# Optimization experiments

Hardware: AMD Instinct MI355X
Metric: run time of the kernel (lower is better)

## Reference

```python
import jax, jax.numpy as jnp
import numpy as np

B, N, H = 32, 1024, 128
EPS = 1e-5


def setup_inputs() -> dict:
    key = jax.random.key(0)
    ks = jax.random.split(key, 9)
    node_embeddings = jax.random.normal(ks[0], (B, N, H), dtype=jnp.float32)
    edge_relations = jax.random.normal(ks[1], (B, N, N, 3), dtype=jnp.float32)
    adjacency = jax.random.randint(ks[2], (N, N), 0, 2, dtype=jnp.int32)
    s_msg = 1.0 / np.sqrt(H + 3)
    s_upd = 1.0 / np.sqrt(2 * H)
    W_msg = jax.random.uniform(ks[3], (H, H + 3), jnp.float32, -s_msg, s_msg)
    b_msg = jax.random.uniform(ks[4], (H,), jnp.float32, -s_msg, s_msg)
    W_upd = jax.random.uniform(ks[5], (H, 2 * H), jnp.float32, -s_upd, s_upd)
    b_upd = jax.random.uniform(ks[6], (H,), jnp.float32, -s_upd, s_upd)
    gamma = jnp.ones((H,), jnp.float32)
    beta = jnp.zeros((H,), jnp.float32)
    return {"node_embeddings": node_embeddings, "edge_relations": edge_relations,
            "adjacency": adjacency, "W_msg": W_msg, "b_msg": b_msg,
            "W_upd": W_upd, "b_upd": b_upd, "gamma": gamma, "beta": beta}


def reference(node_embeddings, edge_relations, adjacency, W_msg, b_msg, W_upd, b_upd, gamma, beta):
    # node_embeddings: [B,N,H]; edge_relations: [B,N,N,3]; adjacency: [N,N]
    b_, n_, h_ = node_embeddings.shape
    mask = (adjacency > 0).astype(node_embeddings.dtype)  # mask[j,i]=1 if i is neighbor of j
    # Split msg_nn weight: Linear(cat(h_i, e_ij)) = h_i @ W_h^T + e_ij @ W_e^T + b
    W_h = W_msg[:, :h_]   # [H,H]
    W_e = W_msg[:, h_:]   # [H,3]
    h_part = jnp.einsum('bih,oh->bio', node_embeddings, W_h)       # [B,N,H]
    msg_h = jnp.einsum('ji,bio->bjo', mask, h_part)                # aggregate sender linear part
    e_agg = jnp.einsum('bijc,ji->bjc', edge_relations, mask)       # aggregate edge feats first (memory-bound)
    msg_e = jnp.einsum('bjc,oc->bjo', e_agg, W_e)
    deg = mask.sum(axis=1)                                         # [N] in-degree of j
    messages = msg_h + msg_e + deg[None, :, None] * b_msg          # bias added once per edge
    # Dropout(0.2) is identity in inference; BatchNorm uses batch stats (training-mode math).
    upd_in = jnp.concatenate([node_embeddings, messages], axis=-1)  # [B,N,2H]
    updated = jax.nn.relu(jnp.einsum('bjk,ok->bjo', upd_in, W_upd) + b_upd)
    flat = updated.reshape(-1, h_)
    mean = flat.mean(axis=0)
    var = flat.var(axis=0)  # biased, as BatchNorm1d
    normed = (flat - mean) * jax.lax.rsqrt(var + EPS) * gamma + beta
    return normed.reshape(b_, n_, h_) + node_embeddings
```

## Files before the change

kernel.cpp:

```cpp
#include <hip/hip_runtime.h>
#include <hip/hip_bf16.h>

typedef _Float16 f16;
typedef f16 f16x4 __attribute__((ext_vector_type(4)));
typedef f16 f16x8 __attribute__((ext_vector_type(8)));
typedef float f32x4 __attribute__((ext_vector_type(4)));

#define BB 32
#define NN 1024
#define HH 128
#define ROWS (BB*NN)
#define EPS 1e-5f

__device__ __forceinline__ f16 f2h(float x) { return (f16)x; }

__global__ __launch_bounds__(256) void prep0_k(
    const float* __restrict__ W_msg, const float* __restrict__ W_upd,
    f16* __restrict__ Wh, f16* __restrict__ Wupd, float* __restrict__ We,
    float* __restrict__ e_agg, float* __restrict__ deg, float* __restrict__ sums)
{
  const int blk = blockIdx.x, t = threadIdx.x;
  if (blk == 0) {
    for (int idx = t; idx < HH*HH; idx += 256) {
      const int o = idx >> 7, h = idx & 127;
      Wh[idx] = f2h(W_msg[o*131 + h]);
    }
  } else if (blk == 1) {
    for (int idx = t; idx < HH*256; idx += 256)
      Wupd[idx] = f2h(W_upd[idx]);
  } else if (blk == 2) {
    for (int idx = t; idx < HH*3; idx += 256)
      We[idx] = W_msg[(idx/3)*131 + 128 + (idx % 3)];
    if (t < 256) sums[t] = 0.f;
    for (int idx = t; idx < NN; idx += 256) deg[idx] = 0.f;
  } else {
    const int base = (blk - 3) * 24576 + t;
    #pragma unroll
    for (int r = 0; r < 96; r++) e_agg[base + r*256] = 0.f;
  }
}

__global__ __launch_bounds__(256) void phaseB_k(
    const float* __restrict__ node, const float* __restrict__ E,
    const int* __restrict__ adj, const f16* __restrict__ Wh,
    f16* __restrict__ h_part_T, float* __restrict__ e_agg,
    float* __restrict__ deg)
{
  __shared__ f16 As[128*32];
  __shared__ f16 Bs[128*32];
  const int tid = threadIdx.x;

  if (blockIdx.x >= 256) {
    const int e  = blockIdx.x - 256;
    const int bb = e >> 5;
    const int r5 = e & 31;
    const int jt = r5 & 3;
    const int ih = r5 >> 2;
    const int j  = (jt << 8) + tid;
    const int i0 = ih << 7;
    const float* Ep = E + (long)bb*3145728 + (long)i0*3072 + (long)j*3;
    const int*   Ap = adj + (long)j*NN + i0;
    float a0 = 0.f, a1 = 0.f, a2 = 0.f, dc = 0.f;
    for (int ii = 0; ii < 128; ii += 8) {
      const int4 m0 = *(const int4*)(Ap + ii);
      const int4 m1 = *(const int4*)(Ap + ii + 4);
      float ev[8][3];
      #pragma unroll
      for (int v = 0; v < 8; v++) {
        const float* q = Ep + (long)(ii + v)*3072;
        ev[v][0] = q[0]; ev[v][1] = q[1]; ev[v][2] = q[2];
      }
      const int mm[8] = {m0.x, m0.y, m0.z, m0.w, m1.x, m1.y, m1.z, m1.w};
      #pragma unroll
      for (int v = 0; v < 8; v++) {
        const float m = (mm[v] > 0) ? 1.f : 0.f;
        a0 = fmaf(m, ev[v][0], a0);
        a1 = fmaf(m, ev[v][1], a1);
        a2 = fmaf(m, ev[v][2], a2);
        dc += m;
      }
    }
    const long eb = ((long)bb*NN + j)*3;
    atomicAdd(&e_agg[eb],     a0);
    atomicAdd(&e_agg[eb + 1], a1);
    atomicAdd(&e_agg[eb + 2], a2);
    if (bb == 0) atomicAdd(&deg[j], dc);
    return;
  }

  const int g  = blockIdx.x;
  const int nt = g & 7, bb = g >> 3;
  const int nbase = nt << 7;
  const int lane = tid & 63, wave = tid >> 6;
  const int wm = (wave & 1) << 6, wn = (wave >> 1) << 6;

  f32x4 acc[2][4];
  #pragma unroll
  for (int i = 0; i < 2; i++)
    #pragma unroll
    for (int j = 0; j < 4; j++)
      #pragma unroll
      for (int r = 0; r < 4; r++) acc[i][j][r] = 0.f;
  f32x4 acc2[2][4];
  #pragma unroll
  for (int i = 0; i < 2; i++)
    #pragma unroll
    for (int j = 0; j < 4; j++)
      #pragma unroll
      for (int r = 0; r < 4; r++) acc2[i][j][r] = 0.f;

  for (int k0 = 0; k0 < HH; k0 += 32) {
    #pragma unroll
    for (int p = 0; p < 2; p++) {
      const int q = (p << 8) + tid;
      const int row = q >> 2, ks = (q & 3) << 3;
      *(uint4*)&As[(row << 5) + ks] = *(const uint4*)&Wh[(long)row*HH + k0 + ks];
    }
    #pragma unroll
    for (int p = 0; p < 4; p++) {
      const int q = (p << 8) + tid;
      const int row = q >> 3, kc = (q & 7) << 2;
      const float4 v = *(const float4*)&node[(long)((bb << 10) + nbase + row)*HH + k0 + kc];
      f16x4 hv; hv[0] = f2h(v.x); hv[1] = f2h(v.y); hv[2] = f2h(v.z); hv[3] = f2h(v.w);
      *(f16x4*)&Bs[(row << 5) + kc] = hv;
    }
    __syncthreads();
    f16x8 af[4], bf[4];
    #pragma unroll
    for (int i = 0; i < 4; i++) {
      af[i] = *(const f16x8*)&As[((wm + (i << 4) + (lane & 15)) << 5) + ((lane >> 4) << 3)];
      bf[i] = *(const f16x8*)&Bs[((wn + (i << 4) + (lane & 15)) << 5) + ((lane >> 4) << 3)];
    }
    #pragma unroll
    for (int i = 0; i < 2; i++)
      #pragma unroll
      for (int j = 0; j < 4; j++) {
        acc[i][j]  = __builtin_amdgcn_mfma_f32_16x16x32_f16(af[i],     bf[j], acc[i][j],  0, 0, 0);
        acc2[i][j] = __builtin_amdgcn_mfma_f32_16x16x32_f16(af[i + 2], bf[j], acc2[i][j], 0, 0, 0);
      }
    __syncthreads();
  }

  f16* out = h_part_T + (long)bb * (HH*NN);
  const int rb = (lane >> 4) << 2, cb = lane & 15;
  #pragma unroll
  for (int i = 0; i < 4; i++)
    #pragma unroll
    for (int r = 0; r < 4; r++) {
      const int gm = wm + (i << 4) + rb + r;
      #pragma unroll
      for (int j = 0; j < 4; j++) {
        const int gn = nbase + wn + (j << 4) + cb;
        const float v = (i < 2) ? acc[i][j][r] : acc2[i - 2][j][r];
        out[(long)gm*NN + gn] = f2h(v);
      }
    }
}

__global__ __launch_bounds__(256) void gemm1_k(
    const int* __restrict__ adj, const f16* __restrict__ hp,
    const float* __restrict__ deg, const float* __restrict__ b_msg,
    const float* __restrict__ e_agg, const float* __restrict__ We,
    f16* __restrict__ msgs)
{
  const int mt = blockIdx.x, bb = blockIdx.z;
  const int jb = mt << 7;
  __shared__ f16 As[128*32];
  __shared__ f16 Bs[128*32];
  const int tid = threadIdx.x, lane = tid & 63, wave = tid >> 6;
  const int wm = (wave & 1) << 6, wn = (wave >> 1) << 6;

  f32x4 acc[4][4];
  #pragma unroll
  for (int i = 0; i < 4; i++)
    #pragma unroll
    for (int j = 0; j < 4; j++)
      #pragma unroll
      for (int r = 0; r < 4; r++) acc[i][j][r] = 0.f;

  for (int k0 = 0; k0 < NN; k0 += 32) {
    #pragma unroll
    for (int p = 0; p < 4; p++) {
      const int q = (p << 8) + tid;
      const int row = q >> 3, kc = (q & 7) << 2;
      const int4 m = *(const int4*)&adj[(long)(jb + row)*NN + k0 + kc];
      f16x4 hv;
      hv[0] = (m.x > 0) ? (f16)1.0f : (f16)0.0f;
      hv[1] = (m.y > 0) ? (f16)1.0f : (f16)0.0f;
      hv[2] = (m.z > 0) ? (f16)1.0f : (f16)0.0f;
      hv[3] = (m.w > 0) ? (f16)1.0f : (f16)0.0f;
      *(f16x4*)&As[(row << 5) + kc] = hv;
    }
    #pragma unroll
    for (int p = 0; p < 2; p++) {
      const int q = (p << 8) + tid;
      const int row = q >> 2, ks = (q & 3) << 3;
      *(uint4*)&Bs[(row << 5) + ks] =
          *(const uint4*)&hp[(long)bb*(HH*NN) + (long)row*NN + k0 + ks];
    }
    __syncthreads();
    f16x8 af[4], bf[4];
    #pragma unroll
    for (int i = 0; i < 4; i++) {
      af[i] = *(const f16x8*)&As[((wm + (i << 4) + (lane & 15)) << 5) + ((lane >> 4) << 3)];
      bf[i] = *(const f16x8*)&Bs[((wn + (i << 4) + (lane & 15)) << 5) + ((lane >> 4) << 3)];
    }
    #pragma unroll
    for (int i = 0; i < 4; i++)
      #pragma unroll
      for (int j = 0; j < 4; j++)
        acc[i][j] = __builtin_amdgcn_mfma_f32_16x16x32_f16(af[i], bf[j], acc[i][j], 0, 0, 0);
    __syncthreads();
  }

  const int rb = (lane >> 4) << 2, cb = lane & 15;
  #pragma unroll
  for (int i = 0; i < 4; i++)
    #pragma unroll
    for (int r = 0; r < 4; r++) {
      const int gm = jb + wm + (i << 4) + rb + r;
      const float dg = deg[gm];
      const long eb = ((long)bb*NN + gm)*3;
      const float e0 = e_agg[eb], e1 = e_agg[eb+1], e2 = e_agg[eb+2];
      #pragma unroll
      for (int j = 0; j < 4; j++) {
        const int gn = wn + (j << 4) + cb;
        const float v = acc[i][j][r] + dg*b_msg[gn]
                      + e0*We[gn*3] + e1*We[gn*3+1] + e2*We[gn*3+2];
        msgs[((long)bb*NN + gm)*HH + gn] = f2h(v);
      }
    }
}

__global__ __launch_bounds__(256) void gemm2_k(
    const float* __restrict__ node, const f16* __restrict__ msgs,
    const f16* __restrict__ Wupd, const float* __restrict__ b_upd,
    f16* __restrict__ upd, float* __restrict__ sums)
{
  const int mt = blockIdx.x;
  const int rowb = mt << 7;
  __shared__ f16 As[128*32];
  __shared__ f16 Bs[128*32];
  __shared__ float colS[128], colQ[128];
  const int tid = threadIdx.x, lane = tid & 63, wave = tid >> 6;
  const int wm = (wave & 1) << 6, wn = (wave >> 1) << 6;
  if (tid < 128) { colS[tid] = 0.f; colQ[tid] = 0.f; }

  f32x4 acc[4][4];
  #pragma unroll
  for (int i = 0; i < 4; i++)
    #pragma unroll
    for (int j = 0; j < 4; j++)
      #pragma unroll
      for (int r = 0; r < 4; r++) acc[i][j][r] = 0.f;

  for (int k0 = 0; k0 < 256; k0 += 32) {
    if (k0 < HH) {
      #pragma unroll
      for (int p = 0; p < 4; p++) {
        const int q = (p << 8) + tid;
        const int row = q >> 3, kc = (q & 7) << 2;
        const float4 v = *(const float4*)&node[(long)(rowb + row)*HH + k0 + kc];
        f16x4 hv; hv[0] = f2h(v.x); hv[1] = f2h(v.y); hv[2] = f2h(v.z); hv[3] = f2h(v.w);
        *(f16x4*)&As[(row << 5) + kc] = hv;
      }
    } else {
      #pragma unroll
      for (int p = 0; p < 2; p++) {
        const int q = (p << 8) + tid;
        const int row = q >> 2, ks = (q & 3) << 3;
        *(uint4*)&As[(row << 5) + ks] =
            *(const uint4*)&msgs[(long)(rowb + row)*HH + (k0 - HH) + ks];
      }
    }
    #pragma unroll
    for (int p = 0; p < 2; p++) {
      const int q = (p << 8) + tid;
      const int row = q >> 2, ks = (q & 3) << 3;
      *(uint4*)&Bs[(row << 5) + ks] = *(const uint4*)&Wupd[(long)row*256 + k0 + ks];
    }
    __syncthreads();
    f16x8 af[4], bf[4];
    #pragma unroll
    for (int i = 0; i < 4; i++) {
      af[i] = *(const f16x8*)&As[((wm + (i << 4) + (lane & 15)) << 5) + ((lane >> 4) << 3)];
      bf[i] = *(const f16x8*)&Bs[((wn + (i << 4) + (lane & 15)) << 5) + ((lane >> 4) << 3)];
    }
    #pragma unroll
    for (int i = 0; i < 4; i++)
      #pragma unroll
      for (int j = 0; j < 4; j++)
        acc[i][j] = __builtin_amdgcn_mfma_f32_16x16x32_f16(af[i], bf[j], acc[i][j], 0, 0, 0);
    __syncthreads();
  }

  const int rb = (lane >> 4) << 2, cb = lane & 15;
  float bup[4], s[4] = {0,0,0,0}, qq[4] = {0,0,0,0};
  #pragma unroll
  for (int j = 0; j < 4; j++) bup[j] = b_upd[wn + (j << 4) + cb];
  #pragma unroll
  for (int i = 0; i < 4; i++)
    #pragma unroll
    for (int r = 0; r < 4; r++) {
      const int gm = rowb + wm + (i << 4) + rb + r;
      #pragma unroll
      for (int j = 0; j < 4; j++) {
        const int gn = wn + (j << 4) + cb;
        const float v = fmaxf(acc[i][j][r] + bup[j], 0.f);
        upd[(long)gm*HH + gn] = f2h(v);
        s[j] += v; qq[j] += v*v;
      }
    }
  #pragma unroll
  for (int j = 0; j < 4; j++) {
    const int gn = wn + (j << 4) + cb;
    atomicAdd(&colS[gn], s[j]);
    atomicAdd(&colQ[gn], qq[j]);
  }
  __syncthreads();
  if (tid < 128) {
    atomicAdd(&sums[tid],       colS[tid]);
    atomicAdd(&sums[128 + tid], colQ[tid]);
  }
}

__global__ __launch_bounds__(256) void final_k(const f16* __restrict__ upd,
    const float* __restrict__ node, const float* __restrict__ sums,
    const float* __restrict__ gamma, const float* __restrict__ beta,
    float* __restrict__ out)
{
  const long idx = (long)blockIdx.x*256 + threadIdx.x;
  const f16x4 u  = *(const f16x4*)&upd[idx << 2];
  const float4 nd = ((const float4*)node)[idx];
  const int ob = (idx & 31) << 2;
  const float inv = 1.0f/32768.0f;
  float4 res;
  #pragma unroll
  for (int c = 0; c < 4; c++) {
    const float m  = sums[ob + c]*inv;
    const float va = sums[128 + ob + c]*inv - m*m;
    const float sc = rsqrtf(va + EPS)*gamma[ob + c];
    ((float*)&res)[c] = ((float)u[c] - m)*sc + beta[ob + c]
                      + ((const float*)&nd)[c];
  }
  ((float4*)out)[idx] = res;
}

extern "C" void kernel_launch(void* const* d_in, const int* in_sizes, int n_in,
                              void* d_out, int out_size, void* d_ws, size_t ws_size,
                              hipStream_t stream) {
  const float* node  = (const float*)d_in[0];
  const float* E     = (const float*)d_in[1];
  const int*   adj   = (const int*)  d_in[2];
  const float* W_msg = (const float*)d_in[3];
  const float* b_msg = (const float*)d_in[4];
  const float* W_upd = (const float*)d_in[5];
  const float* b_upd = (const float*)d_in[6];
  const float* gamma = (const float*)d_in[7];
  const float* beta  = (const float*)d_in[8];
  float* out = (float*)d_out;

  char* p = (char*)d_ws;
  auto alloc = [&](size_t n) { void* r = (void*)p; p += (n + 255) & ~(size_t)255; return r; };
  f16*   h_part_T = (f16*)  alloc((size_t)BB*HH*NN*2);
  f16*   msgs     = (f16*)  alloc((size_t)ROWS*HH*2);
  f16*   upd      = (f16*)  alloc((size_t)ROWS*HH*2);
  float* e_agg    = (float*)alloc((size_t)BB*NN*3*4);
  f16*   Wh       = (f16*)  alloc((size_t)HH*HH*2);
  f16*   Wupd     = (f16*)  alloc((size_t)HH*256*2);
  float* We       = (float*)alloc((size_t)HH*3*4);
  float* deg      = (float*)alloc((size_t)NN*4);
  float* sums     = (float*)alloc((size_t)256*4);

  prep0_k<<<7, 256, 0, stream>>>(W_msg, W_upd, Wh, Wupd, We, e_agg, deg, sums);

  phaseB_k<<<1280, 256, 0, stream>>>(node, E, adj, Wh, h_part_T, e_agg, deg);

  gemm1_k<<<dim3(8, 1, BB), 256, 0, stream>>>(adj, h_part_T, deg, b_msg, e_agg, We, msgs);

  gemm2_k<<<256, 256, 0, stream>>>(node, msgs, Wupd, b_upd, upd, sums);

  final_k<<<4096, 256, 0, stream>>>(upd, node, sums, gamma, beta, out);
}
```

Measured before the change: 653.4 us.

## Precompute fp16 node and mask buffers and load GEMM tiles via global_load_lds

A prep kernel now converts node embeddings to fp16, builds fp16 mask and transposed mask, and computes degree once. The GEMM kernels then load tiles directly into LDS with global_load_lds instead of converting fp32/int data per tile. The edge-aggregation path reads the transposed fp16 mask. This removes repeated conversion work and register staging, at the cost of extra prep work on only a few blocks and additional workspace traffic.

```diff
diff --git a/kernel.cpp b/kernel.cpp
--- a/kernel.cpp
+++ b/kernel.cpp
@@ -1,5 +1,4 @@
 #include <hip/hip_runtime.h>
-#include <hip/hip_bf16.h>
 
 typedef _Float16 f16;
 typedef f16 f16x4 __attribute__((ext_vector_type(4)));
@@ -14,10 +13,18 @@
 
 __device__ __forceinline__ f16 f2h(float x) { return (f16)x; }
 
+typedef __attribute__((address_space(1))) const void gv_t;
+typedef __attribute__((address_space(3))) void lv_t;
+__device__ __forceinline__ void gl_lds16(const void* g, void* l) {
+  __builtin_amdgcn_global_load_lds((gv_t*)g, (lv_t*)l, 16, 0, 0);
+}
+
 __global__ __launch_bounds__(256) void prep0_k(
     const float* __restrict__ W_msg, const float* __restrict__ W_upd,
+    const float* __restrict__ node, const int* __restrict__ adj,
     f16* __restrict__ Wh, f16* __restrict__ Wupd, float* __restrict__ We,
-    float* __restrict__ e_agg, float* __restrict__ deg, float* __restrict__ sums)
+    float* __restrict__ e_agg, float* __restrict__ deg, float* __restrict__ sums,
+    f16* __restrict__ nodeh, f16* __restrict__ maskf, f16* __restrict__ maskT)
 {
   const int blk = blockIdx.x, t = threadIdx.x;
   if (blk == 0) {
@@ -32,19 +39,62 @@
     for (int idx = t; idx < HH*3; idx += 256)
       We[idx] = W_msg[(idx/3)*131 + 128 + (idx % 3)];
     if (t < 256) sums[t] = 0.f;
-    for (int idx = t; idx < NN; idx += 256) deg[idx] = 0.f;
+  } else if (blk < 7) {
+    const int base = (blk - 3) * 24576 + t;
+    #pragma unroll
+    for (int r = 0; r < 96; r++) e_agg[base + r*256] = 0.f;
+  } else if (blk < 15) {
+    __shared__ f16 ldsT[128][136];
+    __shared__ float degl[128];
+    const int tj = blk - 7;
+    if (t < 128) degl[t] = 0.f;
+    __syncthreads();
+    for (int ti = 0; ti < 8; ti++) {
+      #pragma unroll
+      for (int pass = 0; pass < 16; pass++) {
+        const int q = pass*256 + t;
+        const int row = q >> 5, c4 = (q & 31) << 2;
+        const int4 m = *(const int4*)&adj[(long)(tj*128 + row)*NN + ti*128 + c4];
+        f16x4 hv;
+        hv[0] = (m.x > 0) ? (f16)1.0f : (f16)0.0f;
+        hv[1] = (m.y > 0) ? (f16)1.0f : (f16)0.0f;
+        hv[2] = (m.z > 0) ? (f16)1.0f : (f16)0.0f;
+        hv[3] = (m.w > 0) ? (f16)1.0f : (f16)0.0f;
+        *(f16x4*)&maskf[(long)(tj*128 + row)*NN + ti*128 + c4] = hv;
+        ldsT[c4 + 0][row] = hv[0];
+        ldsT[c4 + 1][row] = hv[1];
+        ldsT[c4 + 2][row] = hv[2];
+        ldsT[c4 + 3][row] = hv[3];
+        const int cnt = (m.x > 0) + (m.y > 0) + (m.z > 0) + (m.w > 0);
+        if (cnt) atomicAdd(&degl[row], (float)cnt);
+      }
+      __syncthreads();
+      #pragma unroll
+      for (int pass = 0; pass < 8; pass++) {
+        const int q = pass*256 + t;
+        const int rT = q >> 4, c8 = (q & 15) << 3;
+        *(uint4*)&maskT[(long)(ti*128 + rT)*NN + tj*128 + c8] =
+            *(const uint4*)&ldsT[rT][c8];
+      }
+      __syncthreads();
+    }
+    if (t < 128) deg[tj*128 + t] = degl[t];
   } else {
-    const int base = (blk - 3) * 24576 + t;
-    #pragma unroll
-    for (int r = 0; r < 96; r++) e_agg[base + r*256] = 0.f;
+    const long base = (long)(blk - 15)*256 + t;
+    #pragma unroll
+    for (int p = 0; p < 64; p++) {
+      const long idx = base + (long)p*16384;
+      const float4 v = ((const float4*)node)[idx];
+      f16x4 hv; hv[0] = f2h(v.x); hv[1] = f2h(v.y); hv[2] = f2h(v.z); hv[3] = f2h(v.w);
+      *(f16x4*)&nodeh[idx << 2] = hv;
+    }
   }
 }
 
 __global__ __launch_bounds__(256) void phaseB_k(
-    const float* __restrict__ node, const float* __restrict__ E,
-    const int* __restrict__ adj, const f16* __restrict__ Wh,
-    f16* __restrict__ h_part_T, float* __restrict__ e_agg,
-    float* __restrict__ deg)
+    const f16* __restrict__ nodeh, const float* __restrict__ E,
+    const f16* __restrict__ maskT, const f16* __restrict__ Wh,
+    f16* __restrict__ h_part_T, float* __restrict__ e_agg)
 {
   __shared__ f16 As[128*32];
   __shared__ f16 Bs[128*32];
@@ -59,32 +109,29 @@
     const int j  = (jt << 8) + tid;
     const int i0 = ih << 7;
     const float* Ep = E + (long)bb*3145728 + (long)i0*3072 + (long)j*3;
-    const int*   Ap = adj + (long)j*NN + i0;
-    float a0 = 0.f, a1 = 0.f, a2 = 0.f, dc = 0.f;
+    const f16*   Mp = maskT + (long)i0*NN + j;
+    float a0 = 0.f, a1 = 0.f, a2 = 0.f;
     for (int ii = 0; ii < 128; ii += 8) {
-      const int4 m0 = *(const int4*)(Ap + ii);
-      const int4 m1 = *(const int4*)(Ap + ii + 4);
+      float m[8];
+      #pragma unroll
+      for (int v = 0; v < 8; v++) m[v] = (float)Mp[(long)(ii + v)*NN];
       float ev[8][3];
       #pragma unroll
       for (int v = 0; v < 8; v++) {
         const float* q = Ep + (long)(ii + v)*3072;
         ev[v][0] = q[0]; ev[v][1] = q[1]; ev[v][2] = q[2];
       }
-      const int mm[8] = {m0.x, m0.y, m0.z, m0.w, m1.x, m1.y, m1.z, m1.w};
       #pragma unroll
       for (int v = 0; v < 8; v++) {
-        const float m = (mm[v] > 0) ? 1.f : 0.f;
-        a0 = fmaf(m, ev[v][0], a0);
-        a1 = fmaf(m, ev[v][1], a1);
-        a2 = fmaf(m, ev[v][2], a2);
-        dc += m;
+        a0 = fmaf(m[v], ev[v][0], a0);
+        a1 = fmaf(m[v], ev[v][1], a1);
+        a2 = fmaf(m[v], ev[v][2], a2);
       }
     }
     const long eb = ((long)bb*NN + j)*3;
     atomicAdd(&e_agg[eb],     a0);
     atomicAdd(&e_agg[eb + 1], a1);
     atomicAdd(&e_agg[eb + 2], a2);
-    if (bb == 0) atomicAdd(&deg[j], dc);
     return;
   }
 
@@ -94,35 +141,21 @@
   const int lane = tid & 63, wave = tid >> 6;
   const int wm = (wave & 1) << 6, wn = (wave >> 1) << 6;
 
-  f32x4 acc[2][4];
+  f32x4 acc[2][4], acc2[2][4];
   #pragma unroll
   for (int i = 0; i < 2; i++)
     #pragma unroll
     for (int j = 0; j < 4; j++)
       #pragma unroll
-      for (int r = 0; r < 4; r++) acc[i][j][r] = 0.f;
-  f32x4 acc2[2][4];
-  #pragma unroll
-  for (int i = 0; i < 2; i++)
-    #pragma unroll
-    for (int j = 0; j < 4; j++)
-      #pragma unroll
-      for (int r = 0; r < 4; r++) acc2[i][j][r] = 0.f;
+      for (int r = 0; r < 4; r++) { acc[i][j][r] = 0.f; acc2[i][j][r] = 0.f; }
 
   for (int k0 = 0; k0 < HH; k0 += 32) {
     #pragma unroll
     for (int p = 0; p < 2; p++) {
       const int q = (p << 8) + tid;
-      const int row = q >> 2, ks = (q & 3) << 3;
-      *(uint4*)&As[(row << 5) + ks] = *(const uint4*)&Wh[(long)row*HH + k0 + ks];
-    }
-    #pragma unroll
-    for (int p = 0; p < 4; p++) {
-      const int q = (p << 8) + tid;
-      const int row = q >> 3, kc = (q & 7) << 2;
-      const float4 v = *(const float4*)&node[(long)((bb << 10) + nbase + row)*HH + k0 + kc];
-      f16x4 hv; hv[0] = f2h(v.x); hv[1] = f2h(v.y); hv[2] = f2h(v.z); hv[3] = f2h(v.w);
-      *(f16x4*)&Bs[(row << 5) + kc] = hv;
+      const int row = q >> 2, kp = (q & 3) << 3;
+      gl_lds16(&Wh[(long)row*HH + k0 + kp], &As[q << 3]);
+      gl_lds16(&nodeh[(long)((bb << 10) + nbase + row)*HH + k0 + kp], &Bs[q << 3]);
     }
     __syncthreads();
     f16x8 af[4], bf[4];
@@ -158,7 +191,7 @@
 }
 
 __global__ __launch_bounds__(256) void gemm1_k(
-    const int* __restrict__ adj, const f16* __restrict__ hp,
+    const f16* __restrict__ maskf, const f16* __restrict__ hp,
     const float* __restrict__ deg, const float* __restrict__ b_msg,
     const float* __restrict__ e_agg, const float* __restrict__ We,
     f16* __restrict__ msgs)
@@ -180,23 +213,11 @@
 
   for (int k0 = 0; k0 < NN; k0 += 32) {
     #pragma unroll
-    for (int p = 0; p < 4; p++) {
-      const int q = (p << 8) + tid;
-      const int row = q >> 3, kc = (q & 7) << 2;
-      const int4 m = *(const int4*)&adj[(long)(jb + row)*NN + k0 + kc];
-      f16x4 hv;
-      hv[0] = (m.x > 0) ? (f16)1.0f : (f16)0.0f;
-      hv[1] = (m.y > 0) ? (f16)1.0f : (f16)0.0f;
-      hv[2] = (m.z > 0) ? (f16)1.0f : (f16)0.0f;
-      hv[3] = (m.w > 0) ? (f16)1.0f : (f16)0.0f;
-      *(f16x4*)&As[(row << 5) + kc] = hv;
-    }
-    #pragma unroll
     for (int p = 0; p < 2; p++) {
       const int q = (p << 8) + tid;
-      const int row = q >> 2, ks = (q & 3) << 3;
-      *(uint4*)&Bs[(row << 5) + ks] =
-          *(const uint4*)&hp[(long)bb*(HH*NN) + (long)row*NN + k0 + ks];
+      const int row = q >> 2, kp = (q & 3) << 3;
+      gl_lds16(&maskf[(long)(jb + row)*NN + k0 + kp], &As[q << 3]);
+      gl_lds16(&hp[(long)bb*(HH*NN) + (long)row*NN + k0 + kp], &Bs[q << 3]);
     }
     __syncthreads();
     f16x8 af[4], bf[4];
@@ -233,7 +254,7 @@
 }
 
 __global__ __launch_bounds__(256) void gemm2_k(
-    const float* __restrict__ node, const f16* __restrict__ msgs,
+    const f16* __restrict__ nodeh, const f16* __restrict__ msgs,
     const f16* __restrict__ Wupd, const float* __restrict__ b_upd,
     f16* __restrict__ upd, float* __restrict__ sums)
 {
@@ -255,29 +276,15 @@
       for (int r = 0; r < 4; r++) acc[i][j][r] = 0.f;
 
   for (int k0 = 0; k0 < 256; k0 += 32) {
-    if (k0 < HH) {
-      #pragma unroll
-      for (int p = 0; p < 4; p++) {
-        const int q = (p << 8) + tid;
-        const int row = q >> 3, kc = (q & 7) << 2;
-        const float4 v = *(const float4*)&node[(long)(rowb + row)*HH + k0 + kc];
-        f16x4 hv; hv[0] = f2h(v.x); hv[1] = f2h(v.y); hv[2] = f2h(v.z); hv[3] = f2h(v.w);
-        *(f16x4*)&As[(row << 5) + kc] = hv;
-      }
-    } else {
-      #pragma unroll
-      for (int p = 0; p < 2; p++) {
-        const int q = (p << 8) + tid;
-        const int row = q >> 2, ks = (q & 3) << 3;
-        *(uint4*)&As[(row << 5) + ks] =
-            *(const uint4*)&msgs[(long)(rowb + row)*HH + (k0 - HH) + ks];
-      }
-    }
     #pragma unroll
     for (int p = 0; p < 2; p++) {
       const int q = (p << 8) + tid;
-      const int row = q >> 2, ks = (q & 3) << 3;
-      *(uint4*)&Bs[(row << 5) + ks] = *(const uint4*)&Wupd[(long)row*256 + k0 + ks];
+      const int row = q >> 2, kp = (q & 3) << 3;
+      const f16* src = (k0 < HH)
+        ? &nodeh[(long)(rowb + row)*HH + k0 + kp]
+        : &msgs[(long)(rowb + row)*HH + (k0 - HH) + kp];
+      gl_lds16(src, &As[q << 3]);
+      gl_lds16(&Wupd[(long)row*256 + k0 + kp], &Bs[q << 3]);
     }
     __syncthreads();
     f16x8 af[4], bf[4];
@@ -365,6 +372,9 @@
   f16*   h_part_T = (f16*)  alloc((size_t)BB*HH*NN*2);
   f16*   msgs     = (f16*)  alloc((size_t)ROWS*HH*2);
   f16*   upd      = (f16*)  alloc((size_t)ROWS*HH*2);
+  f16*   nodeh    = (f16*)  alloc((size_t)ROWS*HH*2);
+  f16*   maskf    = (f16*)  alloc((size_t)NN*NN*2);
+  f16*   maskT    = (f16*)  alloc((size_t)NN*NN*2);
   float* e_agg    = (float*)alloc((size_t)BB*NN*3*4);
   f16*   Wh       = (f16*)  alloc((size_t)HH*HH*2);
   f16*   Wupd     = (f16*)  alloc((size_t)HH*256*2);
@@ -372,13 +382,15 @@
   float* deg      = (float*)alloc((size_t)NN*4);
   float* sums     = (float*)alloc((size_t)256*4);
 
-  prep0_k<<<7, 256, 0, stream>>>(W_msg, W_upd, Wh, Wupd, We, e_agg, deg, sums);
-
-  phaseB_k<<<1280, 256, 0, stream>>>(node, E, adj, Wh, h_part_T, e_agg, deg);
-
-  gemm1_k<<<dim3(8, 1, BB), 256, 0, stream>>>(adj, h_part_T, deg, b_msg, e_agg, We, msgs);
-
-  gemm2_k<<<256, 256, 0, stream>>>(node, msgs, Wupd, b_upd, upd, sums);
+  prep0_k<<<79, 256, 0, stream>>>(W_msg, W_upd, node, adj,
+                                  Wh, Wupd, We, e_agg, deg, sums,
+                                  nodeh, maskf, maskT);
+
+  phaseB_k<<<1280, 256, 0, stream>>>(nodeh, E, maskT, Wh, h_part_T, e_agg);
+
+  gemm1_k<<<dim3(8, 1, BB), 256, 0, stream>>>(maskf, h_part_T, deg, b_msg, e_agg, We, msgs);
+
+  gemm2_k<<<256, 256, 0, stream>>>(nodeh, msgs, Wupd, b_upd, upd, sums);
 
   final_k<<<4096, 256, 0, stream>>>(upd, node, sums, gamma, beta, out);
 }
```

New measurement: 690.5 us. 5.7% more time.
